# Performance work log

Measured on AMD Instinct MI355X. Metric: run time of the kernel, lower is better.

Reference implementation:

```python
import jax, jax.numpy as jnp
import numpy as np
import math

B, T, Dm, H = 512, 64, 1024, 16
dh = Dm // H
CD, SD = 32, 256  # smolgen compress_dim, shared_dim
SCALE = 1.0 / math.sqrt(dh)
RES_SCALE = 1.0 / math.sqrt(2.0)  # n_layers=1
EPS = 1e-5


def _ln(v, g, b):
    m = jnp.mean(v, axis=-1, keepdims=True)
    var = jnp.mean(jnp.square(v - m), axis=-1, keepdims=True)
    return (v - m) * jax.lax.rsqrt(var + EPS) * g + b


def setup_inputs() -> dict:
    key = jax.random.key(0)
    ks = jax.random.split(key, 16)
    s = 0.02
    return {
        "x": jax.random.normal(ks[0], (B, T, Dm), jnp.float32),
        # weights stored (in, out); y = x @ W + b
        "Wq": jax.random.normal(ks[1], (Dm, Dm), jnp.float32) * s,
        "Wk": jax.random.normal(ks[2], (Dm, Dm), jnp.float32) * s,
        "Wv": jax.random.normal(ks[3], (Dm, Dm), jnp.float32) * s,
        "Wo_w": jax.random.normal(ks[4], (Dm, Dm), jnp.float32) * s,
        "Wo_b": jnp.zeros((Dm,), jnp.float32),
        "static_bias": jax.random.normal(ks[5], (H, T, T), jnp.float32) * s,
        "aQ": jax.random.normal(ks[6], (H, T, T, dh), jnp.float32) * s,
        "aK": jax.random.normal(ks[7], (H, T, T, dh), jnp.float32) * s,
        "aV": jax.random.normal(ks[8], (H, T, T, dh), jnp.float32) * s,
        # Smolgen params
        "pt_w": jax.random.normal(ks[9], (Dm, CD), jnp.float32) * s,
        "pt_b": jnp.zeros((CD,), jnp.float32),
        "pg_w": jax.random.normal(ks[10], (T * CD, SD), jnp.float32) * s,
        "pg_b": jnp.zeros((SD,), jnp.float32),
        "ph_w": jax.random.normal(ks[11], (SD, H * SD), jnp.float32) * s,
        "ph_b": jnp.zeros((H * SD,), jnp.float32),
        "ln1_g": jnp.ones((SD,), jnp.float32),
        "ln1_b": jnp.zeros((SD,), jnp.float32),
        "ln2_g": jnp.ones((SD,), jnp.float32),
        "ln2_b": jnp.zeros((SD,), jnp.float32),
        "shared_w": jax.random.normal(ks[12], (SD, T * T), jnp.float32) * s,
    }


def _smolgen(x, pt_w, pt_b, pg_w, pg_b, ph_w, ph_b, ln1_g, ln1_b, ln2_g, ln2_b, shared_w):
    z = x @ pt_w + pt_b                      # (B,T,CD)
    g = z.reshape(x.shape[0], T * CD) @ pg_w + pg_b  # (B,SD)
    g = _ln(jax.nn.silu(g), ln1_g, ln1_b)
    u = g @ ph_w + ph_b                      # (B,H*SD)
    u = jax.nn.silu(u).reshape(-1, H, SD)
    u = _ln(u, ln2_g, ln2_b)
    return (u @ shared_w).reshape(-1, H, T, T)


def reference(x, Wq, Wk, Wv, Wo_w, Wo_b, static_bias, aQ, aK, aV,
              pt_w, pt_b, pg_w, pg_b, ph_w, ph_b,
              ln1_g, ln1_b, ln2_g, ln2_b, shared_w):
    Bx = x.shape[0]
    Q = (x @ Wq).reshape(Bx, T, H, dh).transpose(0, 2, 1, 3)  # (B,H,T,dh)
    K = (x @ Wk).reshape(Bx, T, H, dh).transpose(0, 2, 1, 3)
    V = (x @ Wv).reshape(Bx, T, H, dh).transpose(0, 2, 1, 3)
    logits = jnp.einsum('bhtd,bhsd->bhts', Q, K) * SCALE
    logits = logits + static_bias[None]
    logits = logits + jnp.einsum('bhtd,htsd->bhts', Q, aK) * SCALE
    logits = logits + jnp.einsum('htsd,bhsd->bhts', aQ, K) * SCALE
    logits = logits + (jnp.einsum('htsd,htsd->hts', aQ, aK) * SCALE)[None]
    logits = logits + _smolgen(x, pt_w, pt_b, pg_w, pg_b, ph_w, ph_b,
                               ln1_g, ln1_b, ln2_g, ln2_b, shared_w)
    attn = jax.nn.softmax(logits, axis=-1)  # dropout = identity (eval mode)
    out = jnp.einsum('bhts,bhsd->bhtd', attn, V)
    out = out + jnp.einsum('bhts,htsd->bhtd', attn, aV)
    out = out.transpose(0, 2, 1, 3).reshape(Bx, T, Dm)
    return (out @ Wo_w + Wo_b) * RES_SCALE
```

## Files before the change

### kernel.cpp

```cpp
#include <hip/hip_runtime.h>
#include <cstdint>
#include <cstdio>

typedef unsigned short u16;
typedef __attribute__((ext_vector_type(8))) short s8v;
typedef __attribute__((ext_vector_type(4))) float f4v;
typedef __attribute__((ext_vector_type(4))) unsigned short u16x4;
typedef const __attribute__((address_space(1))) void* gas_p;
typedef __attribute__((address_space(3))) void* las_p;

#define DEV __device__ __forceinline__

static constexpr float SCALE_ = 0.125f;
static constexpr float RES_SCALE_ = 0.7071067811865475f;
static constexpr float EPS_ = 1e-5f;

DEV u16 f2bf(float f) {
  uint32_t u = __float_as_uint(f);
  u += 0x7fffu + ((u >> 16) & 1u);
  return (u16)(u >> 16);
}
DEV float bf2f(u16 h) { return __uint_as_float(((uint32_t)h) << 16); }

DEV f4v mfma16(s8v a, s8v b, f4v c) {
  return __builtin_amdgcn_mfma_f32_16x16x32_bf16(a, b, c, 0, 0, 0);
}

#define WAITVM4 asm volatile("s_waitcnt vmcnt(4)" ::: "memory")
#define WAITVM0 asm volatile("s_waitcnt vmcnt(0)" ::: "memory")
#define SCHEDB  __builtin_amdgcn_sched_barrier(0)
#define BAR     __builtin_amdgcn_s_barrier()


__global__ void k_zero(float* __restrict__ p, long n) {
  long i = (long)blockIdx.x * blockDim.x + threadIdx.x;
  long stride = (long)gridDim.x * blockDim.x;
  for (; i < n; i += stride) p[i] = 0.f;
}


DEV void dev_cvt(const float* __restrict__ in, u16* __restrict__ out, long n4,
                 int bid, int nblocks) {
  long i = (long)bid * 256 + threadIdx.x;
  long stride = (long)nblocks * 256;
  for (; i < n4; i += stride) {
    f4v v = *(const f4v*)&in[i * 4];
    u16x4 o;
    o.x = f2bf(v.x); o.y = f2bf(v.y); o.z = f2bf(v.z); o.w = f2bf(v.w);
    *(u16x4*)&out[i * 4] = o;
  }
}

DEV void dev_transpose(const float* __restrict__ in, u16* __restrict__ out,
                       int K, int N, int bx, int by, float tile[64][65]) {
  int kb = bx * 64, nb = by * 64;
  for (int i = threadIdx.x; i < 4096; i += 256) {
    int r = i >> 6, c = i & 63;
    tile[r][c] = in[(long)(kb + r) * N + nb + c];
  }
  __syncthreads();
  for (int i = threadIdx.x; i < 4096; i += 256) {
    int c = i >> 6, r = i & 63;
    out[(long)(nb + c) * K + kb + r] = f2bf(tile[r][c]);
  }
}

DEV void dev_avt(const float* __restrict__ aV, u16* __restrict__ aVt, int ht,
                 float tile[64][65]) {
  const float* src = aV + (long)ht * 4096;
  for (int i = threadIdx.x; i < 4096; i += 256) {
    int s = i >> 6, d = i & 63;
    tile[s][d] = src[i];
  }
  __syncthreads();
  u16* dst = aVt + (long)ht * 4096;
  for (int i = threadIdx.x; i < 4096; i += 256) {
    int d = i >> 6, s = i & 63;
    dst[i] = f2bf(tile[s][d]);
  }
}

__launch_bounds__(256)
__global__ void k_prep(const float* __restrict__ x, u16* __restrict__ xbf,
                       const float* __restrict__ Wq, const float* __restrict__ Wk,
                       const float* __restrict__ Wv, const float* __restrict__ Wo,
                       u16* __restrict__ Wqkvt, u16* __restrict__ Wot,
                       const float* __restrict__ ph_w, u16* __restrict__ phwt,
                       const float* __restrict__ shw, u16* __restrict__ swt,
                       const float* __restrict__ pg_w, u16* __restrict__ pgwT,
                       const float* __restrict__ pt_w, u16* __restrict__ ptwT,
                       const float* __restrict__ aK, u16* __restrict__ aKb,
                       const float* __restrict__ aQ, u16* __restrict__ aQb,
                       const float* __restrict__ aV, u16* __restrict__ aVt,
                       const float* __restrict__ sb, float* __restrict__ extra) {
  __shared__ float tile[64][65];
  int b = blockIdx.x;
  if (b < 2048) { dev_cvt(x, xbf, 8388608, b, 2048); return; }
  b -= 2048;
  if (b < 1024) {
    const float* src = (b < 256) ? Wq : (b < 512) ? Wk : (b < 768) ? Wv : Wo;
    u16* dst = (b < 256) ? Wqkvt : (b < 512) ? (Wqkvt + 1048576)
             : (b < 768) ? (Wqkvt + 2097152) : Wot;
    int id = b & 255;
    dev_transpose(src, dst, 1024, 1024, id & 15, id >> 4, tile);
    return;
  }
  b -= 1024;
  if (b < 256) { dev_transpose(ph_w, phwt, 256, 4096, b & 3, b >> 2, tile); return; }
  b -= 256;
  if (b < 256) { dev_transpose(shw, swt, 256, 4096, b & 3, b >> 2, tile); return; }
  b -= 256;
  if (b < 128) { dev_transpose(pg_w, pgwT, 2048, 256, b & 31, b >> 5, tile); return; }
  b -= 128;
  if (b < 128) {
    int idx = b * 256 + threadIdx.x;
    int n = idx >> 10, k = idx & 1023;
    ptwT[idx] = f2bf(pt_w[k * 32 + n]);
    return;
  }
  b -= 128;
  if (b < 512) { dev_cvt(aK, aKb, 1048576, b, 512); return; }
  b -= 512;
  if (b < 512) { dev_cvt(aQ, aQb, 1048576, b, 512); return; }
  b -= 512;
  if (b < 1024) { dev_avt(aV, aVt, b, tile); return; }
  b -= 1024;
  {
    int idx = b * 256 + threadIdx.x;
    const float* q = aQ + (long)idx * 64;
    const float* k = aK + (long)idx * 64;
    float acc = 0.f;
#pragma unroll 8
    for (int d = 0; d < 64; d++) acc += q[d] * k[d];
    extra[idx] = sb[idx] + acc * SCALE_;
  }
}

template <int EPI>
__launch_bounds__(512)
__global__ void k_gemm256(const u16* __restrict__ A, const u16* __restrict__ Bt,
                          void* __restrict__ Cv, const float* __restrict__ aux,
                          int M, int N, int K) {
  __shared__ u16 lds[65536];

  const int nwg = gridDim.x;
  int wg = blockIdx.x;
  if ((nwg & 7) == 0) wg = (wg & 7) * (nwg >> 3) + (wg >> 3);
  const int ntiles = N >> 8;
  const int mt = wg / ntiles, ntb = wg % ntiles;

  const int tid = threadIdx.x;
  const int lane = tid & 63, w = tid >> 6;
  const int wrB = (w >> 2) * 128, wcB = (w & 3) * 64;
  const int lr = lane & 15, lg = lane >> 4;
  const int hA = w >> 2;
  const int hB = (w & 3) >> 1;
  const int rB0 = (w & 1) * 64;
  const int xs0 = ((lg) ^ (lr & 7)) << 3;
  const int xs1 = ((4 + lg) ^ (lr & 7)) << 3;
  const int nt = K >> 6;

  const int sr = tid >> 3;
  const int sslot = (tid & 7) ^ (sr & 7);

  const u16* aSrc = A + (long)(mt * 256 + sr) * K + sslot * 8;
  const u16* bSrc = Bt + (long)(ntb * 256 + sr) * K + sslot * 8;
  const long h128 = (long)128 * K;
  const long r64 = (long)64 * K;

#define GLOADA(tile, h)                                                          \
  do {                                                                           \
    const int bu_ = (tile) & 1;                                                  \
    const long o_ = (long)(tile) * 64 + (h) * h128;                              \
    __builtin_amdgcn_global_load_lds((gas_p)(aSrc + o_), (las_p)&lds[(bu_ * 2 + (h)) * 8192 + w * 512], 16, 0, 0); \
    __builtin_amdgcn_global_load_lds((gas_p)(aSrc + o_ + r64), (las_p)&lds[(bu_ * 2 + (h)) * 8192 + 4096 + w * 512], 16, 0, 0); \
  } while (0)

#define GLOADB(tile, h)                                                          \
  do {                                                                           \
    const int bu_ = (tile) & 1;                                                  \
    const long o_ = (long)(tile) * 64 + (h) * h128;                              \
    __builtin_amdgcn_global_load_lds((gas_p)(bSrc + o_), (las_p)&lds[32768 + (bu_ * 2 + (h)) * 8192 + w * 512], 16, 0, 0); \
    __builtin_amdgcn_global_load_lds((gas_p)(bSrc + o_ + r64), (las_p)&lds[32768 + (bu_ * 2 + (h)) * 8192 + 4096 + w * 512], 16, 0, 0); \
  } while (0)

  f4v acc[8][4];
#pragma unroll
  for (int mi = 0; mi < 8; mi++)
#pragma unroll
    for (int ni = 0; ni < 4; ni++) acc[mi][ni] = (f4v){0.f, 0.f, 0.f, 0.f};

  GLOADA(0, 0); GLOADA(0, 1);
  GLOADB(0, 0); GLOADB(0, 1);
  {
    const int t1 = (nt > 1) ? 1 : 0;
    GLOADB(t1, 0); GLOADB(t1, 1);
  }
  WAITVM0;
  BAR;

  s8v AF[4][2], b01[2][2], b23[2][2];

  {
    const int aB0 = hA * 8192;
    const int bB0 = 32768 + hB * 8192;
#pragma unroll
    for (int mi = 0; mi < 4; mi++) {
      const int ro = (mi * 16 + lr) * 64;
      AF[mi][0] = *(const s8v*)&lds[aB0 + ro + xs0];
      AF[mi][1] = *(const s8v*)&lds[aB0 + ro + xs1];
    }
#pragma unroll
    for (int ni = 0; ni < 2; ni++) {
      const int ro = (rB0 + ni * 16 + lr) * 64;
      b01[ni][0] = *(const s8v*)&lds[bB0 + ro + xs0];
      b01[ni][1] = *(const s8v*)&lds[bB0 + ro + xs1];
    }
  }
  SCHEDB;

  for (int t = 0; t < nt; ++t) {
    const int p = t & 1, q = p ^ 1;
    const int aN = (t + 1 < nt) ? t + 1 : nt - 1;
    const int bN = (t + 2 < nt) ? t + 2 : nt - 1;
    const int aBase = (p * 2 + hA) * 8192;
    const int bBase = 32768 + (p * 2 + hB) * 8192;
    const int aBaseN = (q * 2 + hA) * 8192;
    const int bBaseN = 32768 + (q * 2 + hB) * 8192;

#pragma unroll
    for (int ni = 0; ni < 2; ni++) {
      const int ro = (rB0 + (2 + ni) * 16 + lr) * 64;
      b23[ni][0] = *(const s8v*)&lds[bBase + ro + xs0];
      b23[ni][1] = *(const s8v*)&lds[bBase + ro + xs1];
    }
    SCHEDB;
    GLOADA(aN, 0);
    BAR;
    __builtin_amdgcn_s_setprio(1);
#pragma unroll
    for (int mi = 0; mi < 4; mi++)
#pragma unroll
      for (int ks = 0; ks < 2; ks++)
#pragma unroll
        for (int ni = 0; ni < 2; ni++)
          acc[mi][ni] = mfma16(AF[mi][ks], b01[ni][ks], acc[mi][ni]);
    __builtin_amdgcn_s_setprio(0);

    GLOADA(aN, 1);
    BAR;
    __builtin_amdgcn_s_setprio(1);
#pragma unroll
    for (int mi = 0; mi < 4; mi++) {
#pragma unroll
      for (int ks = 0; ks < 2; ks++)
#pragma unroll
        for (int ni = 0; ni < 2; ni++)
          acc[mi][2 + ni] = mfma16(AF[mi][ks], b23[ni][ks], acc[mi][2 + ni]);
      const int ro = (64 + mi * 16 + lr) * 64;
      AF[mi][0] = *(const s8v*)&lds[aBase + ro + xs0];
      AF[mi][1] = *(const s8v*)&lds[aBase + ro + xs1];
      SCHEDB;
    }
    __builtin_amdgcn_s_setprio(0);
    BAR;

    GLOADB(bN, 0);
    BAR;
    __builtin_amdgcn_s_setprio(1);
#pragma unroll
    for (int mi = 0; mi < 4; mi++)
#pragma unroll
      for (int ks = 0; ks < 2; ks++)
#pragma unroll
        for (int ni = 0; ni < 2; ni++)
          acc[4 + mi][ni] = mfma16(AF[mi][ks], b01[ni][ks], acc[4 + mi][ni]);
    __builtin_amdgcn_s_setprio(0);

    GLOADB(bN, 1);
    WAITVM4;
    BAR;
#pragma unroll
    for (int ni = 0; ni < 2; ni++) {
      const int ro = (rB0 + ni * 16 + lr) * 64;
      b01[ni][0] = *(const s8v*)&lds[bBaseN + ro + xs0];
      b01[ni][1] = *(const s8v*)&lds[bBaseN + ro + xs1];
    }
    SCHEDB;
    __builtin_amdgcn_s_setprio(1);
#pragma unroll
    for (int mi = 0; mi < 4; mi++) {
#pragma unroll
      for (int ks = 0; ks < 2; ks++)
#pragma unroll
        for (int ni = 0; ni < 2; ni++)
          acc[4 + mi][2 + ni] = mfma16(AF[mi][ks], b23[ni][ks], acc[4 + mi][2 + ni]);
      const int ro = (mi * 16 + lr) * 64;
      AF[mi][0] = *(const s8v*)&lds[aBaseN + ro + xs0];
      AF[mi][1] = *(const s8v*)&lds[aBaseN + ro + xs1];
      SCHEDB;
    }
    __builtin_amdgcn_s_setprio(0);
  }
#undef GLOADA
#undef GLOADB

  const int rbase = mt * 256 + wrB + lg * 4;
  const int cbase = ntb * 256 + wcB + lr;
  if (EPI == 0) {
    u16* C = (u16*)Cv;
#pragma unroll
    for (int mi = 0; mi < 8; mi++)
#pragma unroll
      for (int ni = 0; ni < 4; ni++)
#pragma unroll
        for (int j = 0; j < 4; j++)
          C[(long)(rbase + mi * 16 + j) * N + (cbase + ni * 16)] = f2bf(acc[mi][ni][j]);
  } else if (EPI == 2) {
    u16* C = (u16*)Cv;
#pragma unroll
    for (int mi = 0; mi < 8; mi++)
#pragma unroll
      for (int ni = 0; ni < 4; ni++)
#pragma unroll
        for (int j = 0; j < 4; j++) {
          const int row = rbase + mi * 16 + j;
          const int col = cbase + ni * 16;
          C[(long)row * N + col] = f2bf(acc[mi][ni][j] + aux[((row & 15) << 12) | col]);
        }
  } else {
    float* C = (float*)Cv;
#pragma unroll
    for (int mi = 0; mi < 8; mi++)
#pragma unroll
      for (int ni = 0; ni < 4; ni++)
#pragma unroll
        for (int j = 0; j < 4; j++) {
          const int col = cbase + ni * 16;
          C[(long)(rbase + mi * 16 + j) * N + col] =
              (acc[mi][ni][j] + aux[col]) * RES_SCALE_;
        }
  }
}

template <int EPI>
__launch_bounds__(256)
__global__ void k_gemm(const u16* __restrict__ A, const u16* __restrict__ Bt,
                       void* __restrict__ Cv, const float* __restrict__ aux,
                       int M, int N, int K) {
  __shared__ u16 As[4096];
  __shared__ u16 Bs[4096];
  const int ntiles = N >> 7;
  const int mt = blockIdx.x / ntiles;
  const int nt = blockIdx.x % ntiles;
  const int tid = threadIdx.x;
  const int lane = tid & 63;
  const int w = tid >> 6;
  const int wr = w >> 1, wc = w & 1;
  const int lr = lane & 15, lg = lane >> 4;

  f4v acc[4][4];
#pragma unroll
  for (int m = 0; m < 4; m++)
#pragma unroll
    for (int n = 0; n < 4; n++) acc[m][n] = (f4v){0.f, 0.f, 0.f, 0.f};

  const u16* aSrc = A + (long)(mt * 128 + (tid >> 2)) * K + ((tid & 3) << 3);
  const u16* bSrc = Bt + (long)(nt * 128 + (tid >> 2)) * K + ((tid & 3) << 3);
  const long rowStep = (long)64 * K;

  const int kIters = K >> 5;
  for (int kb = 0; kb < kIters; kb++) {
    if (kb) __syncthreads();
    const u16* aP = aSrc + (kb << 5);
    const u16* bP = bSrc + (kb << 5);
    __builtin_amdgcn_global_load_lds((gas_p)aP, (las_p)&As[w * 512], 16, 0, 0);
    __builtin_amdgcn_global_load_lds((gas_p)(aP + rowStep), (las_p)&As[2048 + w * 512], 16, 0, 0);
    __builtin_amdgcn_global_load_lds((gas_p)bP, (las_p)&Bs[w * 512], 16, 0, 0);
    __builtin_amdgcn_global_load_lds((gas_p)(bP + rowStep), (las_p)&Bs[2048 + w * 512], 16, 0, 0);
    WAITVM0;
    __syncthreads();

    s8v af[4];
#pragma unroll
    for (int m = 0; m < 4; m++)
      af[m] = *(const s8v*)&As[(wr * 64 + m * 16 + lr) * 32 + (lg << 3)];
#pragma unroll
    for (int n = 0; n < 4; n++) {
      s8v bf = *(const s8v*)&Bs[(wc * 64 + n * 16 + lr) * 32 + (lg << 3)];
#pragma unroll
      for (int m = 0; m < 4; m++) acc[m][n] = mfma16(af[m], bf, acc[m][n]);
    }
  }

  const int rbase = mt * 128 + wr * 64 + lg * 4;
  const int cbase = nt * 128 + wc * 64 + lr;
  {
    float* C = (float*)Cv;
#pragma unroll
    for (int m = 0; m < 4; m++)
#pragma unroll
      for (int n = 0; n < 4; n++)
#pragma unroll
        for (int j = 0; j < 4; j++) {
          int row = rbase + m * 16 + j;
          int col = cbase + n * 16;
          C[(long)row * N + col] = acc[m][n][j] + aux[col];
        }
  }
}


__launch_bounds__(256)
__global__ void k_smola_gemm(const u16* __restrict__ xbf, const u16* __restrict__ ptwT,
                             const float* __restrict__ ptb, u16* __restrict__ z) {
  const int rt = blockIdx.x;
  const int w = threadIdx.x >> 6, lane = threadIdx.x & 63;
  const int lr = lane & 15, lg = lane >> 4;
  const int row0 = rt * 64 + w * 16;
  f4v acc[2];
  acc[0] = (f4v){0.f, 0.f, 0.f, 0.f};
  acc[1] = (f4v){0.f, 0.f, 0.f, 0.f};
  const u16* aBase = xbf + (long)(row0 + lr) * 1024;
  const u16* bBase = ptwT + (long)lr * 1024;
#pragma unroll 4
  for (int k0 = 0; k0 < 1024; k0 += 32) {
    s8v a = *(const s8v*)&aBase[k0 + (lg << 3)];
#pragma unroll
    for (int n = 0; n < 2; n++) {
      s8v b = *(const s8v*)&bBase[(long)(n << 4) * 1024 + k0 + (lg << 3)];
      acc[n] = mfma16(a, b, acc[n]);
    }
  }
#pragma unroll
  for (int n = 0; n < 2; n++)
#pragma unroll
    for (int j = 0; j < 4; j++) {
      int col = (n << 4) + lr;
      z[(long)(row0 + lg * 4 + j) * 32 + col] = f2bf(acc[n][j] + ptb[col]);
    }
}

__launch_bounds__(256)
__global__ void k_smolb_ln(const u16* __restrict__ z, const u16* __restrict__ pgwT,
                           const float* __restrict__ pgb, const float* __restrict__ g1,
                           const float* __restrict__ b1, u16* __restrict__ g) {
  __shared__ float tile[16][260];
  const int rt = blockIdx.x;
  const int w = threadIdx.x >> 6, lane = threadIdx.x & 63;
  const int lr = lane & 15, lg = lane >> 4;
  f4v acc[4];
#pragma unroll
  for (int n = 0; n < 4; n++) acc[n] = (f4v){0.f, 0.f, 0.f, 0.f};
  const u16* aBase = z + (long)(rt * 16 + lr) * 2048;
  const u16* bBase = pgwT + (long)(w * 64 + lr) * 2048;
#pragma unroll 4
  for (int k0 = 0; k0 < 2048; k0 += 32) {
    s8v a = *(const s8v*)&aBase[k0 + (lg << 3)];
#pragma unroll
    for (int n = 0; n < 4; n++) {
      s8v b = *(const s8v*)&bBase[(long)(n << 4) * 2048 + k0 + (lg << 3)];
      acc[n] = mfma16(a, b, acc[n]);
    }
  }
#pragma unroll
  for (int n = 0; n < 4; n++)
#pragma unroll
    for (int j = 0; j < 4; j++) {
      int row = lg * 4 + j;
      int col = w * 64 + (n << 4) + lr;
      tile[row][col] = acc[n][j] + pgb[col];
    }
  __syncthreads();
#pragma unroll
  for (int i = 0; i < 4; i++) {
    const int row = w * 4 + i;
    float v[4];
    float s = 0.f, q = 0.f;
#pragma unroll
    for (int j = 0; j < 4; j++) {
      float xx = tile[row][lane * 4 + j];
      v[j] = xx / (1.f + __expf(-xx));
      s += v[j]; q += v[j] * v[j];
    }
#pragma unroll
    for (int mk = 1; mk < 64; mk <<= 1) { s += __shfl_xor(s, mk); q += __shfl_xor(q, mk); }
    float mean = s * (1.f / 256.f);
    float var = q * (1.f / 256.f) - mean * mean;
    float rs = rsqrtf(var + EPS_);
    u16x4 o;
    o.x = f2bf((v[0] - mean) * rs * g1[lane * 4 + 0] + b1[lane * 4 + 0]);
    o.y = f2bf((v[1] - mean) * rs * g1[lane * 4 + 1] + b1[lane * 4 + 1]);
    o.z = f2bf((v[2] - mean) * rs * g1[lane * 4 + 2] + b1[lane * 4 + 2]);
    o.w = f2bf((v[3] - mean) * rs * g1[lane * 4 + 3] + b1[lane * 4 + 3]);
    *(u16x4*)&g[(long)(rt * 16 + row) * 256 + lane * 4] = o;
  }
}

__launch_bounds__(64)
__global__ void k_ln2(const float* __restrict__ uraw, const float* __restrict__ g2,
                      const float* __restrict__ b2, u16* __restrict__ ubf) {
  const int row = blockIdx.x;
  const int lane = threadIdx.x;
  f4v x = *(const f4v*)&uraw[(long)row * 256 + lane * 4];
  float v[4];
  float s = 0.f, q = 0.f;
#pragma unroll
  for (int j = 0; j < 4; j++) {
    float xx = x[j];
    v[j] = xx / (1.f + __expf(-xx));
    s += v[j]; q += v[j] * v[j];
  }
#pragma unroll
  for (int mk = 1; mk < 64; mk <<= 1) { s += __shfl_xor(s, mk); q += __shfl_xor(q, mk); }
  float mean = s * (1.f / 256.f);
  float var = q * (1.f / 256.f) - mean * mean;
  float rs = rsqrtf(var + EPS_);
  u16x4 o;
  float o0 = (v[0] - mean) * rs * g2[lane * 4 + 0] + b2[lane * 4 + 0];
  float o1 = (v[1] - mean) * rs * g2[lane * 4 + 1] + b2[lane * 4 + 1];
  float o2 = (v[2] - mean) * rs * g2[lane * 4 + 2] + b2[lane * 4 + 2];
  float o3 = (v[3] - mean) * rs * g2[lane * 4 + 3] + b2[lane * 4 + 3];
  o.x = f2bf(o0); o.y = f2bf(o1); o.z = f2bf(o2); o.w = f2bf(o3);
  *(u16x4*)&ubf[(long)row * 256 + lane * 4] = o;
}


__launch_bounds__(64)
__global__ void k_l23(const u16* __restrict__ qkv, const u16* __restrict__ aKb,
                      const u16* __restrict__ aQb, u16* __restrict__ l2b,
                      u16* __restrict__ l3a) {
  const int lane = threadIdx.x;
  const int lr = lane & 15, lg = lane >> 4;
  f4v acc[4][4];
#pragma unroll
  for (int m = 0; m < 4; m++)
#pragma unroll
    for (int n = 0; n < 4; n++) acc[m][n] = (f4v){0.f, 0.f, 0.f, 0.f};

  if (blockIdx.x < 8192) {
    const int bid = blockIdx.x;
    const int bt = bid & 7, t = (bid >> 3) & 63, h = bid >> 9;
    const u16* qb = qkv + (long)t * 3072 + h * 64;
    const u16* kb = aKb + ((long)h * 64 + t) * 4096;
#pragma unroll
    for (int ks = 0; ks < 2; ks++) {
      s8v a[4], bb[4];
#pragma unroll
      for (int m = 0; m < 4; m++) {
        int brow = bt * 64 + m * 16 + lr;
        a[m] = *(const s8v*)&qb[(long)brow * 196608 + ks * 32 + (lg << 3)];
      }
#pragma unroll
      for (int n = 0; n < 4; n++)
        bb[n] = *(const s8v*)&kb[(n * 16 + lr) * 64 + ks * 32 + (lg << 3)];
#pragma unroll
      for (int m = 0; m < 4; m++)
#pragma unroll
        for (int n = 0; n < 4; n++) acc[m][n] = mfma16(a[m], bb[n], acc[m][n]);
    }
    u16* dst = l2b + ((long)h * 64 + t) * 32768;
#pragma unroll
    for (int m = 0; m < 4; m++)
#pragma unroll
      for (int n = 0; n < 4; n++)
#pragma unroll
        for (int j = 0; j < 4; j++) {
          int brow = bt * 64 + m * 16 + lg * 4 + j;
          int s = n * 16 + lr;
          dst[(long)brow * 64 + s] = f2bf(SCALE_ * acc[m][n][j]);
        }
  } else {
    const int bid = blockIdx.x - 8192;
    const int bt = bid & 7, s = (bid >> 3) & 63, h = bid >> 9;
    const u16* kb = qkv + (long)s * 3072 + 1024 + h * 64;
    const u16* qb = aQb + (long)h * 262144 + (long)s * 64;
#pragma unroll
    for (int ks = 0; ks < 2; ks++) {
      s8v a[4], bb[4];
#pragma unroll
      for (int m = 0; m < 4; m++) {
        int brow = bt * 64 + m * 16 + lr;
        a[m] = *(const s8v*)&kb[(long)brow * 196608 + ks * 32 + (lg << 3)];
      }
#pragma unroll
      for (int n = 0; n < 4; n++) {
        int tc = n * 16 + lr;
        bb[n] = *(const s8v*)&qb[(long)tc * 4096 + ks * 32 + (lg << 3)];
      }
#pragma unroll
      for (int m = 0; m < 4; m++)
#pragma unroll
        for (int n = 0; n < 4; n++) acc[m][n] = mfma16(a[m], bb[n], acc[m][n]);
    }
#pragma unroll
    for (int m = 0; m < 4; m++)
#pragma unroll
      for (int n = 0; n < 4; n++)
#pragma unroll
        for (int j = 0; j < 4; j++) {
          int brow = bt * 64 + m * 16 + lg * 4 + j;
          int tc = n * 16 + lr;
          long idx = (((long)brow * 16 + h) * 64 + s) * 64 + tc;
          l3a[idx] = f2bf(SCALE_ * acc[m][n][j]);
        }
  }
}

__launch_bounds__(64)
__global__ void k_c(const u16* __restrict__ pbuf, const u16* __restrict__ aVt,
                    u16* __restrict__ outh) {
  const int bid = blockIdx.x;
  const int bt = bid & 7, t = (bid >> 3) & 63, h = bid >> 9;
  const int lane = threadIdx.x;
  const int lr = lane & 15, lg = lane >> 4;
  f4v acc[4][4];
#pragma unroll
  for (int m = 0; m < 4; m++)
#pragma unroll
    for (int n = 0; n < 4; n++) acc[m][n] = (f4v){0.f, 0.f, 0.f, 0.f};
  const u16* ab = pbuf + ((long)h * 64 + t) * 32768 + (long)bt * 4096;
  const u16* vb = aVt + ((long)h * 64 + t) * 4096;
#pragma unroll
  for (int ks = 0; ks < 2; ks++) {
    s8v a[4], bb[4];
#pragma unroll
    for (int m = 0; m < 4; m++)
      a[m] = *(const s8v*)&ab[(m * 16 + lr) * 64 + ks * 32 + (lg << 3)];
#pragma unroll
    for (int n = 0; n < 4; n++)
      bb[n] = *(const s8v*)&vb[(n * 16 + lr) * 64 + ks * 32 + (lg << 3)];
#pragma unroll
    for (int m = 0; m < 4; m++)
#pragma unroll
      for (int n = 0; n < 4; n++) acc[m][n] = mfma16(a[m], bb[n], acc[m][n]);
  }
#pragma unroll
  for (int m = 0; m < 4; m++)
#pragma unroll
    for (int n = 0; n < 4; n++)
#pragma unroll
      for (int j = 0; j < 4; j++) {
        int brow = bt * 64 + m * 16 + lg * 4 + j;
        int d = n * 16 + lr;
        long idx = ((long)brow * 64 + t) * 1024 + h * 64 + d;
        outh[idx] = f2bf(bf2f(outh[idx]) + acc[m][n][j]);
      }
}

__launch_bounds__(256)
__global__ void k_attn(const u16* __restrict__ qkv, const u16* __restrict__ logits,
                       u16* __restrict__ l2b, const u16* __restrict__ l3a,
                       u16* __restrict__ outh) {
  __shared__ u16 Qs[64 * 72];
  __shared__ u16 Ks[64 * 72];
  __shared__ u16 Vt[64 * 72];
  __shared__ u16 Ps[64 * 72];
  const int bh = blockIdx.x;
  const int b = bh >> 4, h = bh & 15;
  const int tid = threadIdx.x;
  const int lane = tid & 63, w = tid >> 6;
  const int lr = lane & 15, lg = lane >> 4;
  const u16* qbase = qkv + (long)b * 196608 + h * 64;

#pragma unroll
  for (int c = 0; c < 2; c++) {
    int flat = c * 2048 + tid * 8;
    int row = flat >> 6, k = flat & 63;
    const u16* src = &qbase[(long)row * 3072 + k];
    *(s8v*)&Qs[row * 72 + k] = *(const s8v*)(src);
    *(s8v*)&Ks[row * 72 + k] = *(const s8v*)(src + 1024);
    s8v v = *(const s8v*)(src + 2048);
#pragma unroll
    for (int j = 0; j < 8; j++) Vt[(k + j) * 72 + row] = (u16)v[j];
  }
  __syncthreads();

  f4v sacc[4];
#pragma unroll
  for (int n = 0; n < 4; n++) sacc[n] = (f4v){0.f, 0.f, 0.f, 0.f};
#pragma unroll
  for (int ks = 0; ks < 2; ks++) {
    s8v a = *(const s8v*)&Qs[(w * 16 + lr) * 72 + ks * 32 + (lg << 3)];
#pragma unroll
    for (int n = 0; n < 4; n++) {
      s8v bb = *(const s8v*)&Ks[(n * 16 + lr) * 72 + ks * 32 + (lg << 3)];
      sacc[n] = mfma16(a, bb, sacc[n]);
    }
  }

  const long base = (long)bh * 4096;
  const int r0 = w * 16 + lg * 4;
  float p[4][4];
#pragma unroll
  for (int n = 0; n < 4; n++) {
    int s = n * 16 + lr;
    u16x4 l3v = *(const u16x4*)&l3a[base + s * 64 + r0];
#pragma unroll
    for (int j = 0; j < 4; j++) {
      float l3f = bf2f(((const u16*)&l3v)[j]);
      float l2f = bf2f(l2b[(((long)h * 64 + r0 + j) * 512 + b) * 64 + s]);
      float lgf = bf2f(logits[base + (r0 + j) * 64 + s]);
      p[n][j] = sacc[n][j] * SCALE_ + lgf + l3f + l2f;
    }
  }
#pragma unroll
  for (int j = 0; j < 4; j++) {
    float m = fmaxf(fmaxf(p[0][j], p[1][j]), fmaxf(p[2][j], p[3][j]));
    m = fmaxf(m, __shfl_xor(m, 1));
    m = fmaxf(m, __shfl_xor(m, 2));
    m = fmaxf(m, __shfl_xor(m, 4));
    m = fmaxf(m, __shfl_xor(m, 8));
    float s0 = 0.f;
#pragma unroll
    for (int n = 0; n < 4; n++) { p[n][j] = __expf(p[n][j] - m); s0 += p[n][j]; }
    s0 += __shfl_xor(s0, 1);
    s0 += __shfl_xor(s0, 2);
    s0 += __shfl_xor(s0, 4);
    s0 += __shfl_xor(s0, 8);
    float inv = 1.f / s0;
#pragma unroll
    for (int n = 0; n < 4; n++) p[n][j] *= inv;
  }

#pragma unroll
  for (int n = 0; n < 4; n++) {
    int s = n * 16 + lr;
#pragma unroll
    for (int j = 0; j < 4; j++) {
      u16 pb = f2bf(p[n][j]);
      l2b[(((long)h * 64 + r0 + j) * 512 + b) * 64 + s] = pb;
      Ps[(r0 + j) * 72 + s] = pb;
    }
  }
  __syncthreads();

  f4v oacc[4];
#pragma unroll
  for (int n = 0; n < 4; n++) oacc[n] = (f4v){0.f, 0.f, 0.f, 0.f};
#pragma unroll
  for (int ks = 0; ks < 2; ks++) {
    s8v a = *(const s8v*)&Ps[(w * 16 + lr) * 72 + ks * 32 + (lg << 3)];
#pragma unroll
    for (int n = 0; n < 4; n++) {
      s8v vb = *(const s8v*)&Vt[(n * 16 + lr) * 72 + ks * 32 + (lg << 3)];
      oacc[n] = mfma16(a, vb, oacc[n]);
    }
  }
  u16* obase = outh + (long)b * 65536 + h * 64;
#pragma unroll
  for (int n = 0; n < 4; n++)
#pragma unroll
    for (int j = 0; j < 4; j++)
      obase[(long)(r0 + j) * 1024 + n * 16 + lr] = f2bf(oacc[n][j]);
}


extern "C" void kernel_launch(void* const* d_in, const int* in_sizes, int n_in,
                              void* d_out, int out_size, void* d_ws, size_t ws_size,
                              hipStream_t stream) {
  (void)in_sizes; (void)n_in;
  const float* x    = (const float*)d_in[0];
  const float* Wq   = (const float*)d_in[1];
  const float* Wk   = (const float*)d_in[2];
  const float* Wv   = (const float*)d_in[3];
  const float* Wo_w = (const float*)d_in[4];
  const float* Wo_b = (const float*)d_in[5];
  const float* sb   = (const float*)d_in[6];
  const float* aQ   = (const float*)d_in[7];
  const float* aK   = (const float*)d_in[8];
  const float* aV   = (const float*)d_in[9];
  const float* pt_w = (const float*)d_in[10];
  const float* pt_b = (const float*)d_in[11];
  const float* pg_w = (const float*)d_in[12];
  const float* pg_b = (const float*)d_in[13];
  const float* ph_w = (const float*)d_in[14];
  const float* ph_b = (const float*)d_in[15];
  const float* ln1g = (const float*)d_in[16];
  const float* ln1b = (const float*)d_in[17];
  const float* ln2g = (const float*)d_in[18];
  const float* ln2b = (const float*)d_in[19];
  const float* shw  = (const float*)d_in[20];

  char* wsp = (char*)d_ws;
  size_t off = 0;
  auto alloc = [&](size_t bytes) {
    void* p = wsp + off;
    off += (bytes + 255) & ~(size_t)255;
    return p;
  };
  u16*   xbf    = (u16*)alloc(33554432ull * 2);
  u16*   qkv    = (u16*)alloc(100663296ull * 2);
  u16*   logits = (u16*)alloc(33554432ull * 2);
  u16*   l3a    = (u16*)alloc(33554432ull * 2);
  u16*   l2b    = (u16*)alloc(33554432ull * 2);
  u16*   Wqkvt  = (u16*)alloc(3145728ull * 2);
  u16*   Wot    = (u16*)alloc(1048576ull * 2);
  u16*   phwt   = (u16*)alloc(1048576ull * 2);
  u16*   swt    = (u16*)alloc(1048576ull * 2);
  u16*   aKb    = (u16*)alloc(4194304ull * 2);
  u16*   aQb    = (u16*)alloc(4194304ull * 2);
  u16*   aVt    = (u16*)alloc(4194304ull * 2);
  float* extra  = (float*)alloc(65536ull * 4);
  u16*   z      = (u16*)alloc(1048576ull * 2);
  u16*   g      = (u16*)alloc(131072ull * 2);
  float* uraw   = (float*)alloc(2097152ull * 4);
  u16*   ubf    = (u16*)alloc(2097152ull * 2);
  u16*   ptwT   = (u16*)alloc(32768ull * 2);
  u16*   pgwT   = (u16*)alloc(524288ull * 2);
  u16*   outh   = xbf;
  float* dout   = (float*)d_out;

  if (off > ws_size) {
    fprintf(stderr, "[kernel_launch] insufficient workspace: need %zu have %zu\n",
            off, ws_size);
    k_zero<<<2048, 256, 0, stream>>>(dout, (long)out_size);
    return;
  }

  k_prep<<<6144, 256, 0, stream>>>(x, xbf, Wq, Wk, Wv, Wo_w, Wqkvt, Wot,
                                   ph_w, phwt, shw, swt, pg_w, pgwT, pt_w, ptwT,
                                   aK, aKb, aQ, aQb, aV, aVt, sb, extra);

  k_gemm256<0><<<1536, 512, 0, stream>>>(xbf, Wqkvt, qkv, nullptr, 32768, 3072, 1024);

  k_l23<<<16384, 64, 0, stream>>>(qkv, aKb, aQb, l2b, l3a);

  k_smola_gemm<<<512, 256, 0, stream>>>(xbf, ptwT, pt_b, z);
  k_smolb_ln<<<32, 256, 0, stream>>>(z, pgwT, pg_b, ln1g, ln1b, g);
  k_gemm<1><<<128, 256, 0, stream>>>(g, phwt, uraw, ph_b, 512, 4096, 256);
  k_ln2<<<8192, 64, 0, stream>>>(uraw, ln2g, ln2b, ubf);
  k_gemm256<2><<<512, 512, 0, stream>>>(ubf, swt, logits, extra, 8192, 4096, 256);

  k_attn<<<8192, 256, 0, stream>>>(qkv, logits, l2b, l3a, outh);
  k_c<<<8192, 64, 0, stream>>>(l2b, aVt, outh);
  k_gemm256<3><<<512, 512, 0, stream>>>(outh, Wot, dout, Wo_b, 32768, 1024, 1024);
}
```

Baseline: 753.2 us.

## Relayout l2/attention-prob buffers to batch-major and pack 4 waves per block

```diff
diff --git a/kernel.cpp b/kernel.cpp
--- a/kernel.cpp
+++ b/kernel.cpp
@@ -475,11 +475,12 @@
 #pragma unroll
   for (int i = 0; i < 4; i++) {
     const int row = w * 4 + i;
+    f4v x = *(const f4v*)&tile[row][lane * 4];
     float v[4];
     float s = 0.f, q = 0.f;
 #pragma unroll
     for (int j = 0; j < 4; j++) {
-      float xx = tile[row][lane * 4 + j];
+      float xx = x[j];
       v[j] = xx / (1.f + __expf(-xx));
       s += v[j]; q += v[j] * v[j];
     }
@@ -497,11 +498,11 @@
   }
 }
 
-__launch_bounds__(64)
+__launch_bounds__(256)
 __global__ void k_ln2(const float* __restrict__ uraw, const float* __restrict__ g2,
                       const float* __restrict__ b2, u16* __restrict__ ubf) {
-  const int row = blockIdx.x;
-  const int lane = threadIdx.x;
+  const int row = blockIdx.x * 4 + (threadIdx.x >> 6);
+  const int lane = threadIdx.x & 63;
   f4v x = *(const f4v*)&uraw[(long)row * 256 + lane * 4];
   float v[4];
   float s = 0.f, q = 0.f;
@@ -526,11 +527,12 @@
 }
 
 
-__launch_bounds__(64)
+__launch_bounds__(256)
 __global__ void k_l23(const u16* __restrict__ qkv, const u16* __restrict__ aKb,
                       const u16* __restrict__ aQb, u16* __restrict__ l2b,
                       u16* __restrict__ l3a) {
-  const int lane = threadIdx.x;
+  const int wid = blockIdx.x * 4 + (threadIdx.x >> 6);
+  const int lane = threadIdx.x & 63;
   const int lr = lane & 15, lg = lane >> 4;
   f4v acc[4][4];
 #pragma unroll
@@ -538,8 +540,8 @@
 #pragma unroll
     for (int n = 0; n < 4; n++) acc[m][n] = (f4v){0.f, 0.f, 0.f, 0.f};
 
-  if (blockIdx.x < 8192) {
-    const int bid = blockIdx.x;
+  if (wid < 8192) {
+    const int bid = wid;
     const int bt = bid & 7, t = (bid >> 3) & 63, h = bid >> 9;
     const u16* qb = qkv + (long)t * 3072 + h * 64;
     const u16* kb = aKb + ((long)h * 64 + t) * 4096;
@@ -559,19 +561,19 @@
 #pragma unroll
         for (int n = 0; n < 4; n++) acc[m][n] = mfma16(a[m], bb[n], acc[m][n]);
     }
-    u16* dst = l2b + ((long)h * 64 + t) * 32768;
+    u16* dst = l2b + ((long)h * 512 + bt * 64) * 4096 + (long)t * 64;
 #pragma unroll
     for (int m = 0; m < 4; m++)
 #pragma unroll
       for (int n = 0; n < 4; n++)
 #pragma unroll
         for (int j = 0; j < 4; j++) {
-          int brow = bt * 64 + m * 16 + lg * 4 + j;
+          int boff = m * 16 + lg * 4 + j;
           int s = n * 16 + lr;
-          dst[(long)brow * 64 + s] = f2bf(SCALE_ * acc[m][n][j]);
+          dst[(long)boff * 4096 + s] = f2bf(SCALE_ * acc[m][n][j]);
         }
   } else {
-    const int bid = blockIdx.x - 8192;
+    const int bid = wid - 8192;
     const int bt = bid & 7, s = (bid >> 3) & 63, h = bid >> 9;
     const u16* kb = qkv + (long)s * 3072 + 1024 + h * 64;
     const u16* qb = aQb + (long)h * 262144 + (long)s * 64;
@@ -607,26 +609,28 @@
   }
 }
 
-__launch_bounds__(64)
-__global__ void k_c(const u16* __restrict__ pbuf, const u16* __restrict__ aVt,
+__launch_bounds__(256)
+__global__ void k_c(const u16* __restrict__ attnb, const u16* __restrict__ aVt,
                     u16* __restrict__ outh) {
-  const int bid = blockIdx.x;
+  const int bid = blockIdx.x * 4 + (threadIdx.x >> 6);
   const int bt = bid & 7, t = (bid >> 3) & 63, h = bid >> 9;
-  const int lane = threadIdx.x;
+  const int lane = threadIdx.x & 63;
   const int lr = lane & 15, lg = lane >> 4;
   f4v acc[4][4];
 #pragma unroll
   for (int m = 0; m < 4; m++)
 #pragma unroll
     for (int n = 0; n < 4; n++) acc[m][n] = (f4v){0.f, 0.f, 0.f, 0.f};
-  const u16* ab = pbuf + ((long)h * 64 + t) * 32768 + (long)bt * 4096;
+  const u16* ab = attnb + ((long)h * 64 + t) * 64;
   const u16* vb = aVt + ((long)h * 64 + t) * 4096;
 #pragma unroll
   for (int ks = 0; ks < 2; ks++) {
     s8v a[4], bb[4];
 #pragma unroll
-    for (int m = 0; m < 4; m++)
-      a[m] = *(const s8v*)&ab[(m * 16 + lr) * 64 + ks * 32 + (lg << 3)];
+    for (int m = 0; m < 4; m++) {
+      int brow = bt * 64 + m * 16 + lr;
+      a[m] = *(const s8v*)&ab[(long)brow * 65536 + ks * 32 + (lg << 3)];
+    }
 #pragma unroll
     for (int n = 0; n < 4; n++)
       bb[n] = *(const s8v*)&vb[(n * 16 + lr) * 64 + ks * 32 + (lg << 3)];
@@ -650,7 +654,7 @@
 
 __launch_bounds__(256)
 __global__ void k_attn(const u16* __restrict__ qkv, const u16* __restrict__ logits,
-                       u16* __restrict__ l2b, const u16* __restrict__ l3a,
+                       const u16* __restrict__ l2b, u16* __restrict__ l3a,
                        u16* __restrict__ outh) {
   __shared__ u16 Qs[64 * 72];
   __shared__ u16 Ks[64 * 72];
@@ -690,6 +694,7 @@
   }
 
   const long base = (long)bh * 4096;
+  const u16* l2base = l2b + ((long)h * 512 + b) * 4096;
   const int r0 = w * 16 + lg * 4;
   float p[4][4];
 #pragma unroll
@@ -699,7 +704,7 @@
 #pragma unroll
     for (int j = 0; j < 4; j++) {
       float l3f = bf2f(((const u16*)&l3v)[j]);
-      float l2f = bf2f(l2b[(((long)h * 64 + r0 + j) * 512 + b) * 64 + s]);
+      float l2f = bf2f(l2base[(r0 + j) * 64 + s]);
       float lgf = bf2f(logits[base + (r0 + j) * 64 + s]);
       p[n][j] = sacc[n][j] * SCALE_ + lgf + l3f + l2f;
     }
@@ -723,13 +728,15 @@
     for (int n = 0; n < 4; n++) p[n][j] *= inv;
   }
 
+  __syncthreads();
+
 #pragma unroll
   for (int n = 0; n < 4; n++) {
     int s = n * 16 + lr;
 #pragma unroll
     for (int j = 0; j < 4; j++) {
       u16 pb = f2bf(p[n][j]);
-      l2b[(((long)h * 64 + r0 + j) * 512 + b) * 64 + s] = pb;
+      l3a[base + (r0 + j) * 64 + s] = pb;
       Ps[(r0 + j) * 72 + s] = pb;
     }
   }
@@ -824,15 +831,14 @@
 
   k_gemm256<0><<<1536, 512, 0, stream>>>(xbf, Wqkvt, qkv, nullptr, 32768, 3072, 1024);
 
-  k_l23<<<16384, 64, 0, stream>>>(qkv, aKb, aQb, l2b, l3a);
-
   k_smola_gemm<<<512, 256, 0, stream>>>(xbf, ptwT, pt_b, z);
   k_smolb_ln<<<32, 256, 0, stream>>>(z, pgwT, pg_b, ln1g, ln1b, g);
   k_gemm<1><<<128, 256, 0, stream>>>(g, phwt, uraw, ph_b, 512, 4096, 256);
-  k_ln2<<<8192, 64, 0, stream>>>(uraw, ln2g, ln2b, ubf);
+  k_ln2<<<2048, 256, 0, stream>>>(uraw, ln2g, ln2b, ubf);
   k_gemm256<2><<<512, 512, 0, stream>>>(ubf, swt, logits, extra, 8192, 4096, 256);
 
+  k_l23<<<4096, 256, 0, stream>>>(qkv, aKb, aQb, l2b, l3a);
   k_attn<<<8192, 256, 0, stream>>>(qkv, logits, l2b, l3a, outh);
-  k_c<<<8192, 64, 0, stream>>>(l2b, aVt, outh);
+  k_c<<<2048, 256, 0, stream>>>(l3a, aVt, outh);
   k_gemm256<3><<<512, 512, 0, stream>>>(outh, Wot, dout, Wo_b, 32768, 1024, 1024);
 }
```

After: 762.1 us. Within noise of the previous version (+1.2%).
